# Optimization experiments

Measured on AMD Instinct MI355X. Metric: run time of the kernel, lower is better.

## Reference

```python
import jax, jax.numpy as jnp
import numpy as np

# SMPL-X mesh sizes; BVH padded collision-pair count P = F * max_collisions
B, NV, F, MAXC = 16, 10475, 20908, 8
P = F * MAXC
SIGMA = 0.001          # distance-field cone height (df_cone_height)
LINEAR_MAX = 1000.0    # linear cap on penetration depth
PENALIZE_OUTSIDE = True  # module config: DistanceFieldPenetrationLoss(penalize_outside=True)


def setup_inputs() -> dict:
    key = jax.random.key(0)
    k1, k2, k3, k4 = jax.random.split(key, 4)
    # body-model output vertices (B, NV, 3)
    v = jax.random.normal(k1, (B, NV, 3), dtype=jnp.float32) * 0.5
    # triangle vertex indices (F, 3)
    faces = jax.random.randint(k2, (F, 3), 0, NV, dtype=jnp.int64)
    # BVH output: padded (intruder, receiver) triangle-index pairs per batch elem,
    # -1 marks invalid (padding) slots, as torch-mesh-isect's BVH emits.
    collision_idxs = jax.random.randint(k3, (B, P, 2), 0, F, dtype=jnp.int64)
    invalid = jax.random.uniform(k4, (B, P, 1)) < 0.75
    collision_idxs = jnp.where(invalid, jnp.int64(-1), collision_idxs)
    return {"v": v, "faces": faces, "collision_idxs": collision_idxs}


def pen_distance(triangles, collision_idxs):
    """Distance-field penetration loss over collision pairs.

    triangles: (B, F, 3, 3); collision_idxs: (B, P, 2) with -1 = invalid pair.
    Returns per-batch loss (B,).
    """
    mask = jnp.all(collision_idxs >= 0, axis=-1)          # (B, P)
    idx = jnp.maximum(collision_idxs, 0)
    # gather intruding / receiving triangles: (B, P, 3, 3)
    intr = jnp.take_along_axis(triangles, idx[..., 0][:, :, None, None], axis=1)
    recv = jnp.take_along_axis(triangles, idx[..., 1][:, :, None, None], axis=1)

    # receiver conic distance field: centroid + unit normal
    c = recv.mean(axis=-2)                                 # (B, P, 3)
    n = jnp.cross(recv[..., 1, :] - recv[..., 0, :],
                  recv[..., 2, :] - recv[..., 0, :])
    n = n / (jnp.linalg.norm(n, axis=-1, keepdims=True) + 1e-12)

    u = intr - c[..., None, :]                             # (B, P, 3v, 3c)
    # signed penetration depth of each intruder vertex (positive = behind plane)
    t = -jnp.einsum('bpvc,bpc->bpv', u, n)                 # (B, P, 3)
    depth = jnp.clip(t, 0.0, LINEAR_MAX)

    if not PENALIZE_OUTSIDE:
        # radial attenuation inside a cone of height SIGMA over the triangle
        radial = jnp.linalg.norm(u + t[..., None] * n[..., None, :], axis=-1)
        r_base = jnp.linalg.norm(recv - c[..., None, :], axis=-1).max(axis=-1)
        cone_r = r_base[..., None] * jnp.clip(1.0 - t / SIGMA, 0.0, 1.0)
        depth = depth * jax.nn.relu(1.0 - radial / (cone_r + 1e-12))

    psi2 = jnp.sum(depth * depth, axis=-1)                 # (B, P)
    return jnp.sum(jnp.where(mask, psi2, 0.0), axis=-1)   # (B,)


def reference(v, faces, collision_idxs):
    # triangles = v.view(-1,3)[faces_ids] : per-batch triangle vertex gather
    triangles = v[:, faces]                                # (B, F, 3, 3)
    # BVH search ran under torch.no_grad(); indices are constants here
    collision_idxs = jax.lax.stop_gradient(collision_idxs)
    return pen_distance(triangles, collision_idxs)
```

## Files before the change

### kernel.cpp

```cpp
#include <hip/hip_runtime.h>

constexpr int B_  = 16;
constexpr int NV_ = 10475;
constexpr int F_  = 20908;
constexpr int P_  = F_ * 8;
constexpr int BF_ = B_ * F_;
constexpr float LINEAR_MAX_ = 1000.0f;


__global__ __launch_bounds__(256) void face_precompute_kernel(
    const float* __restrict__ v,
    const int*   __restrict__ faces,
    float4*      __restrict__ cnd,
    float4*      __restrict__ verts)
{
    const int f = blockIdx.x * blockDim.x + threadIdx.x;
    const int b = blockIdx.y;
    if (f >= F_) return;

    const float* __restrict__ vb = v + (size_t)b * (NV_ * 3);
    const int i0 = faces[f * 3 + 0] * 3;
    const int i1 = faces[f * 3 + 1] * 3;
    const int i2 = faces[f * 3 + 2] * 3;

    const float v0x = vb[i0 + 0], v0y = vb[i0 + 1], v0z = vb[i0 + 2];
    const float v1x = vb[i1 + 0], v1y = vb[i1 + 1], v1z = vb[i1 + 2];
    const float v2x = vb[i2 + 0], v2y = vb[i2 + 1], v2z = vb[i2 + 2];

    const float third = 1.0f / 3.0f;
    const float cx = (v0x + v1x + v2x) * third;
    const float cy = (v0y + v1y + v2y) * third;
    const float cz = (v0z + v1z + v2z) * third;

    const float e1x = v1x - v0x, e1y = v1y - v0y, e1z = v1z - v0z;
    const float e2x = v2x - v0x, e2y = v2y - v0y, e2z = v2z - v0z;
    float nx = e1y * e2z - e1z * e2y;
    float ny = e1z * e2x - e1x * e2z;
    float nz = e1x * e2y - e1y * e2x;
    const float inv = 1.0f / (sqrtf(nx * nx + ny * ny + nz * nz) + 1e-12f);
    nx *= inv; ny *= inv; nz *= inv;

    const int bf = b * F_ + f;
    cnd[bf] = make_float4(nx, ny, nz, cx * nx + cy * ny + cz * nz);
    verts[bf * 3 + 0] = make_float4(v0x, v0y, v0z, v1x);
    verts[bf * 3 + 1] = make_float4(v1y, v1z, v2x, v2y);
    verts[bf * 3 + 2] = make_float4(v2z, 0.0f, 0.0f, 0.0f);
}

__global__ __launch_bounds__(256) void pen_pairs_kernel(
    const int2*  __restrict__ coll,
    const float4* __restrict__ cnd,
    const float4* __restrict__ verts,
    float*       __restrict__ out)
{
    const int p = blockIdx.x * blockDim.x + threadIdx.x;
    const int b = blockIdx.y;

    float psi2 = 0.0f;

    if (p < F_) {
        const int2* __restrict__ cb = coll + (size_t)b * P_ + p;
        const int bofs = b * F_;

        #pragma unroll
        for (int k = 0; k < 8; ++k) {
            const int2 pr = cb[k * F_];
            const float m = ((pr.x | pr.y) >= 0) ? 1.0f : 0.0f;
            const int fR = bofs + ((pr.y > 0) ? pr.y : 0);
            const int fI = bofs + ((pr.x > 0) ? pr.x : 0);

            const float4 nd = cnd[fR];
            const float4 L0 = verts[fI * 3 + 0];
            const float4 L1 = verts[fI * 3 + 1];
            const float4 L2 = verts[fI * 3 + 2];

            float s = 0.0f;
            float t0 = nd.w - (L0.x * nd.x + L0.y * nd.y + L0.z * nd.z);
            t0 = fminf(fmaxf(t0, 0.0f), LINEAR_MAX_);
            s = fmaf(t0, t0, s);
            float t1 = nd.w - (L0.w * nd.x + L1.x * nd.y + L1.y * nd.z);
            t1 = fminf(fmaxf(t1, 0.0f), LINEAR_MAX_);
            s = fmaf(t1, t1, s);
            float t2 = nd.w - (L1.z * nd.x + L1.w * nd.y + L2.x * nd.z);
            t2 = fminf(fmaxf(t2, 0.0f), LINEAR_MAX_);
            s = fmaf(t2, t2, s);

            psi2 = fmaf(m, s, psi2);
        }
    }

    #pragma unroll
    for (int off = 32; off > 0; off >>= 1)
        psi2 += __shfl_down(psi2, off, 64);

    __shared__ float wsum[4];
    const int lane = threadIdx.x & 63;
    const int wid  = threadIdx.x >> 6;
    if (lane == 0) wsum[wid] = psi2;
    __syncthreads();

    if (threadIdx.x == 0) {
        const float blocksum = wsum[0] + wsum[1] + wsum[2] + wsum[3];
        atomicAdd(&out[b], blocksum);
    }
}

extern "C" void kernel_launch(void* const* d_in, const int* in_sizes, int n_in,
                              void* d_out, int out_size, void* d_ws, size_t ws_size,
                              hipStream_t stream) {
    const float* v     = (const float*)d_in[0];
    const int*   faces = (const int*)d_in[1];
    const int2*  coll  = (const int2*)d_in[2];
    float* out = (float*)d_out;

    float4* cnd   = (float4*)d_ws;
    float4* verts = (float4*)((char*)d_ws + (size_t)BF_ * sizeof(float4));

    hipMemsetAsync(out, 0, out_size * sizeof(float), stream);

    dim3 block(256);
    dim3 gridA((F_ + 255) / 256, B_);
    face_precompute_kernel<<<gridA, block, 0, stream>>>(v, faces, cnd, verts);

    dim3 gridB((F_ + 255) / 256, B_);
    pen_pairs_kernel<<<gridB, block, 0, stream>>>(coll, cnd, verts, out);
}
```

Before: 106.7 us.

## Gather intruder vertices from packed vertex array and swizzle blocks across XCDs

Stops materializing per-face vertex triples (48B/face/batch) and instead packs vertices into float4 and faces into int4, so the pair kernel gathers intruder vertices through face indices from a much smaller per-batch vertex array that is more likely to stay cache-resident. Grids are flattened and remapped so that each batch's blocks land on a consistent XCD, improving L2 locality for that batch's cnd and vertex data. The cost is an extra kernel launch and an extra level of dependent indirection (face index, then vertex) in the hot loop.

```diff
diff --git a/kernel.cpp b/kernel.cpp
--- a/kernel.cpp
+++ b/kernel.cpp
@@ -8,80 +8,105 @@
 constexpr float LINEAR_MAX_ = 1000.0f;
 
 
-__global__ __launch_bounds__(256) void face_precompute_kernel(
+__device__ __forceinline__ void swz(int bid, int& b, int& px) {
+    const int xcd = bid & 7;
+    const int j   = bid >> 3;
+    b  = xcd + ((j & 1) << 3);
+    px = j >> 1;
+}
+
+__global__ __launch_bounds__(256) void pre_pack_kernel(
     const float* __restrict__ v,
     const int*   __restrict__ faces,
-    float4*      __restrict__ cnd,
-    float4*      __restrict__ verts)
+    float4*      __restrict__ vpack,
+    int4*        __restrict__ faces4)
 {
-    const int f = blockIdx.x * blockDim.x + threadIdx.x;
-    const int b = blockIdx.y;
+    const int bid = blockIdx.x;
+    int b, px; swz(bid, b, px);
+    const int t = threadIdx.x;
+
+    const int g = bid * 256 + t;
+    if (g < F_)
+        faces4[g] = make_int4(faces[g*3+0], faces[g*3+1], faces[g*3+2], 0);
+
+    const int vid = px * 256 + t;
+    if (vid < NV_) {
+        const float* src = v + ((size_t)b * NV_ + vid) * 3;
+        vpack[b * NV_ + vid] = make_float4(src[0], src[1], src[2], 0.0f);
+    }
+}
+
+__global__ __launch_bounds__(256) void face_cnd_kernel(
+    const float4* __restrict__ vpack,
+    const int4*   __restrict__ faces4,
+    float4*       __restrict__ cnd)
+{
+    const int bid = blockIdx.x;
+    int b, px; swz(bid, b, px);
+    const int f = px * 256 + threadIdx.x;
     if (f >= F_) return;
 
-    const float* __restrict__ vb = v + (size_t)b * (NV_ * 3);
-    const int i0 = faces[f * 3 + 0] * 3;
-    const int i1 = faces[f * 3 + 1] * 3;
-    const int i2 = faces[f * 3 + 2] * 3;
-
-    const float v0x = vb[i0 + 0], v0y = vb[i0 + 1], v0z = vb[i0 + 2];
-    const float v1x = vb[i1 + 0], v1y = vb[i1 + 1], v1z = vb[i1 + 2];
-    const float v2x = vb[i2 + 0], v2y = vb[i2 + 1], v2z = vb[i2 + 2];
+    const int4 fi = faces4[f];
+    const float4* vb = vpack + (size_t)b * NV_;
+    const float4 p0 = vb[fi.x];
+    const float4 p1 = vb[fi.y];
+    const float4 p2 = vb[fi.z];
 
     const float third = 1.0f / 3.0f;
-    const float cx = (v0x + v1x + v2x) * third;
-    const float cy = (v0y + v1y + v2y) * third;
-    const float cz = (v0z + v1z + v2z) * third;
+    const float cx = (p0.x + p1.x + p2.x) * third;
+    const float cy = (p0.y + p1.y + p2.y) * third;
+    const float cz = (p0.z + p1.z + p2.z) * third;
 
-    const float e1x = v1x - v0x, e1y = v1y - v0y, e1z = v1z - v0z;
-    const float e2x = v2x - v0x, e2y = v2y - v0y, e2z = v2z - v0z;
+    const float e1x = p1.x - p0.x, e1y = p1.y - p0.y, e1z = p1.z - p0.z;
+    const float e2x = p2.x - p0.x, e2y = p2.y - p0.y, e2z = p2.z - p0.z;
     float nx = e1y * e2z - e1z * e2y;
     float ny = e1z * e2x - e1x * e2z;
     float nz = e1x * e2y - e1y * e2x;
     const float inv = 1.0f / (sqrtf(nx * nx + ny * ny + nz * nz) + 1e-12f);
     nx *= inv; ny *= inv; nz *= inv;
 
-    const int bf = b * F_ + f;
-    cnd[bf] = make_float4(nx, ny, nz, cx * nx + cy * ny + cz * nz);
-    verts[bf * 3 + 0] = make_float4(v0x, v0y, v0z, v1x);
-    verts[bf * 3 + 1] = make_float4(v1y, v1z, v2x, v2y);
-    verts[bf * 3 + 2] = make_float4(v2z, 0.0f, 0.0f, 0.0f);
+    cnd[b * F_ + f] = make_float4(nx, ny, nz, cx * nx + cy * ny + cz * nz);
 }
 
 __global__ __launch_bounds__(256) void pen_pairs_kernel(
-    const int2*  __restrict__ coll,
+    const int2*   __restrict__ coll,
     const float4* __restrict__ cnd,
-    const float4* __restrict__ verts,
-    float*       __restrict__ out)
+    const float4* __restrict__ vpack,
+    const int4*   __restrict__ faces4,
+    float*        __restrict__ out)
 {
-    const int p = blockIdx.x * blockDim.x + threadIdx.x;
-    const int b = blockIdx.y;
+    const int bid = blockIdx.x;
+    int b, px; swz(bid, b, px);
+    const int p = px * 256 + threadIdx.x;
 
     float psi2 = 0.0f;
 
     if (p < F_) {
         const int2* __restrict__ cb = coll + (size_t)b * P_ + p;
-        const int bofs = b * F_;
+        const float4* __restrict__ vb = vpack + (size_t)b * NV_;
+        const float4* __restrict__ cb_cnd = cnd + (size_t)b * F_;
 
         #pragma unroll
         for (int k = 0; k < 8; ++k) {
             const int2 pr = cb[k * F_];
             const float m = ((pr.x | pr.y) >= 0) ? 1.0f : 0.0f;
-            const int fR = bofs + ((pr.y > 0) ? pr.y : 0);
-            const int fI = bofs + ((pr.x > 0) ? pr.x : 0);
+            const int fR = (pr.y > 0) ? pr.y : 0;
+            const int fI = (pr.x > 0) ? pr.x : 0;
 
-            const float4 nd = cnd[fR];
-            const float4 L0 = verts[fI * 3 + 0];
-            const float4 L1 = verts[fI * 3 + 1];
-            const float4 L2 = verts[fI * 3 + 2];
+            const float4 nd = cb_cnd[fR];
+            const int4   fi = faces4[fI];
+            const float4 a0 = vb[fi.x];
+            const float4 a1 = vb[fi.y];
+            const float4 a2 = vb[fi.z];
 
             float s = 0.0f;
-            float t0 = nd.w - (L0.x * nd.x + L0.y * nd.y + L0.z * nd.z);
+            float t0 = nd.w - (a0.x * nd.x + a0.y * nd.y + a0.z * nd.z);
             t0 = fminf(fmaxf(t0, 0.0f), LINEAR_MAX_);
             s = fmaf(t0, t0, s);
-            float t1 = nd.w - (L0.w * nd.x + L1.x * nd.y + L1.y * nd.z);
+            float t1 = nd.w - (a1.x * nd.x + a1.y * nd.y + a1.z * nd.z);
             t1 = fminf(fmaxf(t1, 0.0f), LINEAR_MAX_);
             s = fmaf(t1, t1, s);
-            float t2 = nd.w - (L1.z * nd.x + L1.w * nd.y + L2.x * nd.z);
+            float t2 = nd.w - (a2.x * nd.x + a2.y * nd.y + a2.z * nd.z);
             t2 = fminf(fmaxf(t2, 0.0f), LINEAR_MAX_);
             s = fmaf(t2, t2, s);
 
@@ -113,15 +138,15 @@
     const int2*  coll  = (const int2*)d_in[2];
     float* out = (float*)d_out;
 
-    float4* cnd   = (float4*)d_ws;
-    float4* verts = (float4*)((char*)d_ws + (size_t)BF_ * sizeof(float4));
+    char* ws = (char*)d_ws;
+    float4* cnd    = (float4*)ws;                                  ws += (size_t)BF_ * 16;
+    float4* vpack  = (float4*)ws;                                  ws += (size_t)B_ * NV_ * 16;
+    int4*   faces4 = (int4*)ws;
 
     hipMemsetAsync(out, 0, out_size * sizeof(float), stream);
 
     dim3 block(256);
-    dim3 gridA((F_ + 255) / 256, B_);
-    face_precompute_kernel<<<gridA, block, 0, stream>>>(v, faces, cnd, verts);
-
-    dim3 gridB((F_ + 255) / 256, B_);
-    pen_pairs_kernel<<<gridB, block, 0, stream>>>(coll, cnd, verts, out);
+    pre_pack_kernel<<<dim3(656), block, 0, stream>>>(v, faces, vpack, faces4);
+    face_cnd_kernel<<<dim3(1312), block, 0, stream>>>(vpack, faces4, cnd);
+    pen_pairs_kernel<<<dim3(1312), block, 0, stream>>>(coll, cnd, vpack, faces4, out);
 }
```

New measurement: 101.4 us. 1.05x faster.

## Interleave face records into 64B table, swizzle blocks per XCD, one pair per thread

Applied to the files above, without the earlier changes.

Merges the plane and vertex arrays into one 64-byte record per face. It also remaps block IDs so that each XCD handles one or two batch elements, keeping that batch's face table in its local L2. The pair kernel now handles one collision pair per thread over all P pairs instead of looping eight per thread. The goal is better L2 locality for the random gathers and more parallelism, at the cost of 8x more blocks and atomics, plus a larger and partly wasted record footprint.

```diff
diff --git a/kernel.cpp b/kernel.cpp
--- a/kernel.cpp
+++ b/kernel.cpp
@@ -8,14 +8,20 @@
 constexpr float LINEAR_MAX_ = 1000.0f;
 
 
-__global__ __launch_bounds__(256) void face_precompute_kernel(
+__device__ __forceinline__ void swz(int bid, int& b, int& px) {
+    const int xcd = bid & 7;
+    const int j   = bid >> 3;
+    b  = xcd + ((j & 1) << 3);
+    px = j >> 1;
+}
+
+__global__ __launch_bounds__(256) void face_rec_kernel(
     const float* __restrict__ v,
     const int*   __restrict__ faces,
-    float4*      __restrict__ cnd,
-    float4*      __restrict__ verts)
+    float4*      __restrict__ tbl)
 {
-    const int f = blockIdx.x * blockDim.x + threadIdx.x;
-    const int b = blockIdx.y;
+    int b, px; swz(blockIdx.x, b, px);
+    const int f = px * 256 + threadIdx.x;
     if (f >= F_) return;
 
     const float* __restrict__ vb = v + (size_t)b * (NV_ * 3);
@@ -40,53 +46,47 @@
     const float inv = 1.0f / (sqrtf(nx * nx + ny * ny + nz * nz) + 1e-12f);
     nx *= inv; ny *= inv; nz *= inv;
 
-    const int bf = b * F_ + f;
-    cnd[bf] = make_float4(nx, ny, nz, cx * nx + cy * ny + cz * nz);
-    verts[bf * 3 + 0] = make_float4(v0x, v0y, v0z, v1x);
-    verts[bf * 3 + 1] = make_float4(v1y, v1z, v2x, v2y);
-    verts[bf * 3 + 2] = make_float4(v2z, 0.0f, 0.0f, 0.0f);
+    float4* rec = tbl + ((size_t)b * F_ + f) * 4;
+    rec[0] = make_float4(nx, ny, nz, cx * nx + cy * ny + cz * nz);
+    rec[1] = make_float4(v0x, v0y, v0z, v1x);
+    rec[2] = make_float4(v1y, v1z, v2x, v2y);
+    rec[3] = make_float4(v2z, 0.0f, 0.0f, 0.0f);
 }
 
 __global__ __launch_bounds__(256) void pen_pairs_kernel(
-    const int2*  __restrict__ coll,
-    const float4* __restrict__ cnd,
-    const float4* __restrict__ verts,
-    float*       __restrict__ out)
+    const int2*   __restrict__ coll,
+    const float4* __restrict__ tbl,
+    float*        __restrict__ out)
 {
-    const int p = blockIdx.x * blockDim.x + threadIdx.x;
-    const int b = blockIdx.y;
+    int b, px; swz(blockIdx.x, b, px);
+    const int p = px * 256 + threadIdx.x;
 
     float psi2 = 0.0f;
 
-    if (p < F_) {
-        const int2* __restrict__ cb = coll + (size_t)b * P_ + p;
-        const int bofs = b * F_;
+    if (p < P_) {
+        const int2 pr = coll[(size_t)b * P_ + p];
+        const float m = ((pr.x | pr.y) >= 0) ? 1.0f : 0.0f;
+        const int fR = (pr.y > 0) ? pr.y : 0;
+        const int fI = (pr.x > 0) ? pr.x : 0;
 
-        #pragma unroll
-        for (int k = 0; k < 8; ++k) {
-            const int2 pr = cb[k * F_];
-            const float m = ((pr.x | pr.y) >= 0) ? 1.0f : 0.0f;
-            const int fR = bofs + ((pr.y > 0) ? pr.y : 0);
-            const int fI = bofs + ((pr.x > 0) ? pr.x : 0);
+        const float4* __restrict__ bt = tbl + (size_t)b * F_ * 4;
+        const float4 nd = bt[fR * 4 + 0];
+        const float4 L0 = bt[fI * 4 + 1];
+        const float4 L1 = bt[fI * 4 + 2];
+        const float4 L2 = bt[fI * 4 + 3];
 
-            const float4 nd = cnd[fR];
-            const float4 L0 = verts[fI * 3 + 0];
-            const float4 L1 = verts[fI * 3 + 1];
-            const float4 L2 = verts[fI * 3 + 2];
+        float s = 0.0f;
+        float t0 = nd.w - (L0.x * nd.x + L0.y * nd.y + L0.z * nd.z);
+        t0 = fminf(fmaxf(t0, 0.0f), LINEAR_MAX_);
+        s = fmaf(t0, t0, s);
+        float t1 = nd.w - (L0.w * nd.x + L1.x * nd.y + L1.y * nd.z);
+        t1 = fminf(fmaxf(t1, 0.0f), LINEAR_MAX_);
+        s = fmaf(t1, t1, s);
+        float t2 = nd.w - (L1.z * nd.x + L1.w * nd.y + L2.x * nd.z);
+        t2 = fminf(fmaxf(t2, 0.0f), LINEAR_MAX_);
+        s = fmaf(t2, t2, s);
 
-            float s = 0.0f;
-            float t0 = nd.w - (L0.x * nd.x + L0.y * nd.y + L0.z * nd.z);
-            t0 = fminf(fmaxf(t0, 0.0f), LINEAR_MAX_);
-            s = fmaf(t0, t0, s);
-            float t1 = nd.w - (L0.w * nd.x + L1.x * nd.y + L1.y * nd.z);
-            t1 = fminf(fmaxf(t1, 0.0f), LINEAR_MAX_);
-            s = fmaf(t1, t1, s);
-            float t2 = nd.w - (L1.z * nd.x + L1.w * nd.y + L2.x * nd.z);
-            t2 = fminf(fmaxf(t2, 0.0f), LINEAR_MAX_);
-            s = fmaf(t2, t2, s);
-
-            psi2 = fmaf(m, s, psi2);
-        }
+        psi2 = m * s;
     }
 
     #pragma unroll
@@ -112,16 +112,11 @@
     const int*   faces = (const int*)d_in[1];
     const int2*  coll  = (const int2*)d_in[2];
     float* out = (float*)d_out;
-
-    float4* cnd   = (float4*)d_ws;
-    float4* verts = (float4*)((char*)d_ws + (size_t)BF_ * sizeof(float4));
+    float4* tbl = (float4*)d_ws;
 
     hipMemsetAsync(out, 0, out_size * sizeof(float), stream);
 
     dim3 block(256);
-    dim3 gridA((F_ + 255) / 256, B_);
-    face_precompute_kernel<<<gridA, block, 0, stream>>>(v, faces, cnd, verts);
-
-    dim3 gridB((F_ + 255) / 256, B_);
-    pen_pairs_kernel<<<gridB, block, 0, stream>>>(coll, cnd, verts, out);
+    face_rec_kernel<<<dim3(1312), block, 0, stream>>>(v, faces, tbl);
+    pen_pairs_kernel<<<dim3(10464), block, 0, stream>>>(coll, tbl, out);
 }
```

Result: slower. 218.9 us (+105.1%).
